# Kernel optimization log

Measured on AMD Instinct MI355X. Metric: run time of the kernel, lower is better.

Reference implementation:

```python
import jax, jax.numpy as jnp
import numpy as np

N_NODES = 100000
N_EDGES = 600000
IN_CH = 128
HID = 64
N_REL = 8


def setup_inputs() -> dict:
    key = jax.random.key(0)
    ks = jax.random.split(key, 9)
    x = jax.random.normal(ks[0], (N_NODES, IN_CH), dtype=jnp.float32)
    edge_index = jax.random.randint(ks[1], (2, N_EDGES), 0, N_NODES)
    edge_type = jax.random.randint(ks[2], (N_EDGES,), 0, N_REL)
    s_in = 1.0 / np.sqrt(IN_CH)   # torch Linear init bound
    s_h = 1.0 / np.sqrt(HID)
    W_rel = jax.random.uniform(ks[3], (N_REL, HID, IN_CH), minval=-s_in, maxval=s_in, dtype=jnp.float32)
    b_rel = jax.random.uniform(ks[4], (N_REL, HID), minval=-s_in, maxval=s_in, dtype=jnp.float32)
    W_self = jax.random.uniform(ks[5], (HID, IN_CH), minval=-s_in, maxval=s_in, dtype=jnp.float32)
    b_self = jax.random.uniform(ks[6], (HID,), minval=-s_in, maxval=s_in, dtype=jnp.float32)
    W_out = jax.random.uniform(ks[7], (1, HID), minval=-s_h, maxval=s_h, dtype=jnp.float32)
    b_out = jax.random.uniform(ks[8], (1,), minval=-s_h, maxval=s_h, dtype=jnp.float32)
    return {"x": x, "edge_index": edge_index, "edge_type": edge_type,
            "W_rel": W_rel, "b_rel": b_rel, "W_self": W_self, "b_self": b_self,
            "W_out": W_out, "b_out": b_out}


def reference(x, edge_index, edge_type, W_rel, b_rel, W_self, b_self, W_out, b_out):
    row, col = edge_index[0], edge_index[1]
    R, H, _ = W_rel.shape
    N = x.shape[0]
    # Project every node under every relation once ([R, N, H]) instead of the
    # per-relation masked gather->GEMM loop: same math (sum over edges of
    # W_{edge_type} x_{src} + b_{edge_type} scattered into dst).
    xp = jnp.einsum('ni,rhi->rnh', x, W_rel)                     # [R, N, H]
    msg = xp.reshape(R * N, H)[edge_type * N + row] + b_rel[edge_type]  # [E, H]
    agg = jax.ops.segment_sum(msg, col, num_segments=N)          # scatter-add into dst
    out = jax.nn.relu(agg + x @ W_self.T + b_self)               # [N, H]
    return (out @ W_out.T + b_out)[:, 0]                          # [N]
```

## Files before the change

### kernel.cpp

```cpp
#include <hip/hip_runtime.h>
#include <hip/hip_bf16.h>

#define IN_CH    128
#define HID      64
#define N_REL    8
#define KSTEP    36
#define SROW2    580
#define SLOT_CAP 64

using bf16x8 = __attribute__((ext_vector_type(8))) short;
using f32x4  = __attribute__((ext_vector_type(4))) float;

__device__ __forceinline__ short f2bf(float f) {
    unsigned int u = __float_as_uint(f);
    u += 0x7fffu + ((u >> 16) & 1u);
    return (short)(u >> 16);
}

__global__ __launch_bounds__(256) void prep_fill_kernel(
    const float* __restrict__ x, unsigned short* __restrict__ xb, int total8,
    const float* __restrict__ W_rel, const float* __restrict__ W_self,
    unsigned short* __restrict__ wpk,
    const int* __restrict__ edge_index, const int* __restrict__ edge_type,
    int* __restrict__ cnt, unsigned int* __restrict__ slots, int E, int nb_xb)
{
    const int b = blockIdx.x, tid = threadIdx.x;
    if (b < nb_xb) {
        int i = b * 256 + tid;
        if (i >= total8) return;
        const float* p = x + (size_t)i * 8;
        float4 a = *(const float4*)p;
        float4 c = *(const float4*)(p + 4);
        bf16x8 o;
        o[0]=f2bf(a.x); o[1]=f2bf(a.y); o[2]=f2bf(a.z); o[3]=f2bf(a.w);
        o[4]=f2bf(c.x); o[5]=f2bf(c.y); o[6]=f2bf(c.z); o[7]=f2bf(c.w);
        *(bf16x8*)(xb + (size_t)i * 8) = o;
    } else if (b < nb_xb + 36) {
        int gid = (b - nb_xb) * 256 + tid;
        int s2   = gid >> 8;
        int t    = (gid >> 6) & 3;
        int lane = gid & 63;
        int h    = t * 16 + (lane & 15);
        int kb   = s2 * 32 + (lane >> 4) * 8;
        bf16x8 o;
        #pragma unroll
        for (int j = 0; j < 8; ++j) {
            int k = kb + j;
            float v = (k < 1024)
                ? W_rel[(size_t)(k >> 7) * HID * IN_CH + (size_t)h * IN_CH + (k & 127)]
                : W_self[(size_t)h * IN_CH + (k - 1024)];
            o[j] = f2bf(v);
        }
        *(bf16x8*)(wpk + (size_t)gid * 8) = o;
    } else {
        int e = (b - nb_xb - 36) * 256 + tid;
        if (e >= E) return;
        int dst = edge_index[E + e];
        unsigned int src = (unsigned int)edge_index[e];
        unsigned int t   = (unsigned int)edge_type[e];
        int pos = atomicAdd(&cnt[dst], 1);
        if (pos < SLOT_CAP)
            slots[(size_t)dst * SLOT_CAP + pos] = (src << 8) | (t << 28);
    }
}

__global__ __launch_bounds__(1024, 8) void rgcn_fused_kernel(
    const unsigned int* __restrict__ xbu,
    const unsigned short* __restrict__ wpk,
    const int* __restrict__ cnt,
    const unsigned int* __restrict__ slots,
    const float* __restrict__ b_rel,
    const float* __restrict__ b_self,
    const float* __restrict__ W_out,
    const float* __restrict__ b_out,
    float* __restrict__ out,
    int N)
{
    __shared__ unsigned int Sb[16 * SROW2];
    __shared__ int cntS[16 * 8];
    const int tid  = threadIdx.x;
    const int wave = tid >> 6;
    const int lane = tid & 63;
    const int l16  = lane & 15;
    const int quad = lane >> 4;
    const int nb   = blockIdx.x * 16;
    const int gnode = nb + wave;

    const unsigned int selfv = xbu[(size_t)gnode * 64 + lane];
    const int rawdeg = cnt[gnode];
    const unsigned int ev = slots[(size_t)gnode * SLOT_CAP + lane];

    #pragma unroll
    for (int k = 0; k < 8; ++k) {
        int idx = k * 1024 + tid;
        Sb[(idx >> 9) * SROW2 + (idx & 511)] = 0;
    }

    const int deg = (rawdeg > SLOT_CAP) ? SLOT_CAP : rawdeg;
    const int myr = (lane < deg) ? (int)(ev >> 28) : 8;
    const unsigned long long below =
        (lane == 63) ? 0x7FFFFFFFFFFFFFFFull : ((1ull << lane) - 1ull);
    int rank = 0, off = 0;
    #pragma unroll
    for (int r = 0; r < 8; ++r) {
        unsigned long long m = __ballot(myr == r);
        int c = __popcll(m);
        if (lane == 0) cntS[wave * 8 + r] = c;
        if (myr == r) rank = off + (int)__popcll(m & below);
        off += c;
    }
    {
        unsigned long long minv = __ballot(myr == 8);
        if (myr == 8) rank = off + (int)__popcll(minv & below);
    }
    const int evs = __builtin_amdgcn_ds_permute(rank << 2, (int)ev);

    __syncthreads();

    {
        const char* xbase = (const char*)xbu + (lane << 2);
        unsigned int* Srow = &Sb[wave * SROW2];
        float s0 = 0.f, s1 = 0.f;
        int cur_r = -1;
        for (int e0 = 0; e0 < deg; e0 += 8) {
            int bn = deg - e0; if (bn > 8) bn = 8;
            unsigned int vv[8], uu[8];
            #pragma unroll
            for (int i = 0; i < 8; ++i) {
                if (i < bn) {
                    vv[i] = (unsigned int)__shfl(evs, e0 + i, 64);
                    uu[i] = *(const unsigned int*)(xbase + (vv[i] & 0x0FFFFFFFu));
                }
            }
            #pragma unroll
            for (int i = 0; i < 8; ++i) {
                if (i >= bn) break;
                const int r = __builtin_amdgcn_readfirstlane((int)(vv[i] >> 28));
                if (r != cur_r) {
                    if (cur_r >= 0) {
                        unsigned int p =
                            ((unsigned int)(unsigned short)f2bf(s1) << 16)
                          | (unsigned int)(unsigned short)f2bf(s0);
                        Srow[cur_r * 64 + lane] = p;
                    }
                    cur_r = r; s0 = 0.f; s1 = 0.f;
                }
                s0 += __uint_as_float(uu[i] << 16);
                s1 += __uint_as_float(uu[i] & 0xffff0000u);
            }
        }
        if (cur_r >= 0) {
            unsigned int p = ((unsigned int)(unsigned short)f2bf(s1) << 16)
                           | (unsigned int)(unsigned short)f2bf(s0);
            Srow[cur_r * 64 + lane] = p;
        }
        Srow[512 + lane] = selfv;
    }
    __syncthreads();

    f32x4 acc[4] = {{0.f,0.f,0.f,0.f},{0.f,0.f,0.f,0.f},
                    {0.f,0.f,0.f,0.f},{0.f,0.f,0.f,0.f}};
    if (wave < 8) {
        const bf16x8* wv = (const bf16x8*)wpk;
        const int s0w = (wave < 4) ? wave * 5 : 20 + (wave - 4) * 4;
        const int ns  = (wave < 4) ? 5 : 4;
        for (int q = 0; q < ns; ++q) {
            const int s2 = s0w + q;
            bf16x8 a[4];
            #pragma unroll
            for (int t = 0; t < 4; ++t)
                a[t] = wv[(size_t)((s2 * 4 + t) * 64) + lane];
            bf16x8 bfrag = *(const bf16x8*)&Sb[l16 * SROW2 + s2 * 16 + quad * 4];
            #pragma unroll
            for (int t = 0; t < 4; ++t)
                acc[t] = __builtin_amdgcn_mfma_f32_16x16x32_bf16(
                    a[t], bfrag, acc[t], 0, 0, 0);
        }
    }
    __syncthreads();

    float* Pf = (float*)Sb;
    if (wave < 8) {
        #pragma unroll
        for (int t = 0; t < 4; ++t)
            *(f32x4*)&Pf[wave * 1100 + l16 * 68 + t * 16 + quad * 4] = acc[t];
    }
    __syncthreads();

    if (tid < 256) {
        const int node = tid & 15, hg = tid >> 4;
        f32x4 v = {0.f, 0.f, 0.f, 0.f};
        #pragma unroll
        for (int w2 = 0; w2 < 8; ++w2)
            v += *(const f32x4*)&Pf[w2 * 1100 + node * 68 + hg * 4];
        float4 bs = *(const float4*)(b_self + hg * 4);
        float4 wo = *(const float4*)(W_out + hg * 4);
        float cb[4] = {0.f, 0.f, 0.f, 0.f};
        #pragma unroll
        for (int r = 0; r < 8; ++r) {
            float cf = (float)cntS[node * 8 + r];
            if (cf != 0.f) {
                float4 br = *(const float4*)(b_rel + r * HID + hg * 4);
                cb[0] += cf * br.x; cb[1] += cf * br.y;
                cb[2] += cf * br.z; cb[3] += cf * br.w;
            }
        }
        float part = 0.f;
        #pragma unroll
        for (int j = 0; j < 4; ++j) {
            float u = v[j] + (&bs.x)[j] + cb[j];
            u = fmaxf(u, 0.f);
            part += u * (&wo.x)[j];
        }
        Pf[8800 + hg * 16 + node] = part;
    }
    __syncthreads();
    if (tid < 16) {
        float sum = 0.f;
        #pragma unroll
        for (int hg = 0; hg < 16; ++hg) sum += Pf[8800 + hg * 16 + tid];
        out[nb + tid] = sum + b_out[0];
    }
}

extern "C" void kernel_launch(void* const* d_in, const int* in_sizes, int n_in,
                              void* d_out, int out_size, void* d_ws, size_t ws_size,
                              hipStream_t stream)
{
    const float* x          = (const float*)d_in[0];
    const int*   edge_index = (const int*)  d_in[1];
    const int*   edge_type  = (const int*)  d_in[2];
    const float* W_rel      = (const float*)d_in[3];
    const float* b_rel      = (const float*)d_in[4];
    const float* W_self     = (const float*)d_in[5];
    const float* b_self     = (const float*)d_in[6];
    const float* W_out      = (const float*)d_in[7];
    const float* b_out      = (const float*)d_in[8];
    float* out = (float*)d_out;

    const int N = in_sizes[0] / IN_CH;
    const int E = in_sizes[2];

    char* w = (char*)d_ws;
    unsigned short* xb  = (unsigned short*)w;  w += (size_t)N * IN_CH * 2;
    unsigned short* wpk = (unsigned short*)w;  w += (size_t)KSTEP * 4 * 64 * 8 * 2;
    int* cnt            = (int*)w;             w += (size_t)N * 4;
    unsigned int* slots = (unsigned int*)w;    w += (size_t)N * SLOT_CAP * 4;

    const int total8 = N * IN_CH / 8;
    const int nb_xb  = (total8 + 255) / 256;
    const int nb_e   = (E + 255) / 256;

    hipMemsetAsync(cnt, 0, (size_t)N * 4, stream);

    prep_fill_kernel<<<nb_xb + 36 + nb_e, 256, 0, stream>>>(
        x, xb, total8, W_rel, W_self, wpk,
        edge_index, edge_type, cnt, slots, E, nb_xb);

    rgcn_fused_kernel<<<N / 16, 1024, 0, stream>>>(
        (const unsigned int*)xb, wpk, cnt, slots,
        b_rel, b_self, W_out, b_out, out, N);
}
```

Baseline: 240.8 us.

## Drop bf16 pre-conversion of x and gather fp32 rows directly

Removes the prep pass that converted all of x to bf16. The fused kernel now gathers neighbor rows as fp32 float2 straight from x and converts the self row to bf16 in-kernel. Slot encoding shifts src by 9 so it becomes a byte offset into 512-byte fp32 rows. Edge loads and slot stores are marked nontemporal. This saves a full read/write pass over x, but each gather now moves twice the bytes, and src<<9 caps the node index at 2^19 before it collides with the type bits.

```diff
diff --git a/kernel.cpp b/kernel.cpp
--- a/kernel.cpp
+++ b/kernel.cpp
@@ -18,25 +18,14 @@
 }
 
 __global__ __launch_bounds__(256) void prep_fill_kernel(
-    const float* __restrict__ x, unsigned short* __restrict__ xb, int total8,
     const float* __restrict__ W_rel, const float* __restrict__ W_self,
     unsigned short* __restrict__ wpk,
     const int* __restrict__ edge_index, const int* __restrict__ edge_type,
-    int* __restrict__ cnt, unsigned int* __restrict__ slots, int E, int nb_xb)
+    int* __restrict__ cnt, unsigned int* __restrict__ slots, int E)
 {
     const int b = blockIdx.x, tid = threadIdx.x;
-    if (b < nb_xb) {
-        int i = b * 256 + tid;
-        if (i >= total8) return;
-        const float* p = x + (size_t)i * 8;
-        float4 a = *(const float4*)p;
-        float4 c = *(const float4*)(p + 4);
-        bf16x8 o;
-        o[0]=f2bf(a.x); o[1]=f2bf(a.y); o[2]=f2bf(a.z); o[3]=f2bf(a.w);
-        o[4]=f2bf(c.x); o[5]=f2bf(c.y); o[6]=f2bf(c.z); o[7]=f2bf(c.w);
-        *(bf16x8*)(xb + (size_t)i * 8) = o;
-    } else if (b < nb_xb + 36) {
-        int gid = (b - nb_xb) * 256 + tid;
+    if (b < 36) {
+        int gid = b * 256 + tid;
         int s2   = gid >> 8;
         int t    = (gid >> 6) & 3;
         int lane = gid & 63;
@@ -53,19 +42,20 @@
         }
         *(bf16x8*)(wpk + (size_t)gid * 8) = o;
     } else {
-        int e = (b - nb_xb - 36) * 256 + tid;
+        int e = (b - 36) * 256 + tid;
         if (e >= E) return;
-        int dst = edge_index[E + e];
-        unsigned int src = (unsigned int)edge_index[e];
-        unsigned int t   = (unsigned int)edge_type[e];
+        int dst = __builtin_nontemporal_load(edge_index + E + e);
+        unsigned int src = (unsigned int)__builtin_nontemporal_load(edge_index + e);
+        unsigned int t   = (unsigned int)__builtin_nontemporal_load(edge_type + e);
         int pos = atomicAdd(&cnt[dst], 1);
         if (pos < SLOT_CAP)
-            slots[(size_t)dst * SLOT_CAP + pos] = (src << 8) | (t << 28);
+            __builtin_nontemporal_store((src << 9) | (t << 28),
+                                        &slots[(size_t)dst * SLOT_CAP + pos]);
     }
 }
 
 __global__ __launch_bounds__(1024, 8) void rgcn_fused_kernel(
-    const unsigned int* __restrict__ xbu,
+    const float* __restrict__ x,
     const unsigned short* __restrict__ wpk,
     const int* __restrict__ cnt,
     const unsigned int* __restrict__ slots,
@@ -86,7 +76,7 @@
     const int nb   = blockIdx.x * 16;
     const int gnode = nb + wave;
 
-    const unsigned int selfv = xbu[(size_t)gnode * 64 + lane];
+    const float2 sf = *(const float2*)((const char*)x + (size_t)gnode * 512 + (lane << 3));
     const int rawdeg = cnt[gnode];
     const unsigned int ev = slots[(size_t)gnode * SLOT_CAP + lane];
 
@@ -118,18 +108,19 @@
     __syncthreads();
 
     {
-        const char* xbase = (const char*)xbu + (lane << 2);
+        const char* xbase = (const char*)x + (lane << 3);
         unsigned int* Srow = &Sb[wave * SROW2];
         float s0 = 0.f, s1 = 0.f;
         int cur_r = -1;
         for (int e0 = 0; e0 < deg; e0 += 8) {
             int bn = deg - e0; if (bn > 8) bn = 8;
-            unsigned int vv[8], uu[8];
+            unsigned int vv[8];
+            float2 uu[8];
             #pragma unroll
             for (int i = 0; i < 8; ++i) {
                 if (i < bn) {
                     vv[i] = (unsigned int)__shfl(evs, e0 + i, 64);
-                    uu[i] = *(const unsigned int*)(xbase + (vv[i] & 0x0FFFFFFFu));
+                    uu[i] = *(const float2*)(xbase + (vv[i] & 0x07FFFFFFu));
                 }
             }
             #pragma unroll
@@ -145,8 +136,8 @@
                     }
                     cur_r = r; s0 = 0.f; s1 = 0.f;
                 }
-                s0 += __uint_as_float(uu[i] << 16);
-                s1 += __uint_as_float(uu[i] & 0xffff0000u);
+                s0 += uu[i].x;
+                s1 += uu[i].y;
             }
         }
         if (cur_r >= 0) {
@@ -154,7 +145,8 @@
                            | (unsigned int)(unsigned short)f2bf(s0);
             Srow[cur_r * 64 + lane] = p;
         }
-        Srow[512 + lane] = selfv;
+        Srow[512 + lane] = ((unsigned int)(unsigned short)f2bf(sf.y) << 16)
+                         | (unsigned int)(unsigned short)f2bf(sf.x);
     }
     __syncthreads();
 
@@ -242,22 +234,17 @@
     const int E = in_sizes[2];
 
     char* w = (char*)d_ws;
-    unsigned short* xb  = (unsigned short*)w;  w += (size_t)N * IN_CH * 2;
     unsigned short* wpk = (unsigned short*)w;  w += (size_t)KSTEP * 4 * 64 * 8 * 2;
     int* cnt            = (int*)w;             w += (size_t)N * 4;
     unsigned int* slots = (unsigned int*)w;    w += (size_t)N * SLOT_CAP * 4;
 
-    const int total8 = N * IN_CH / 8;
-    const int nb_xb  = (total8 + 255) / 256;
-    const int nb_e   = (E + 255) / 256;
+    const int nb_e = (E + 255) / 256;
 
     hipMemsetAsync(cnt, 0, (size_t)N * 4, stream);
 
-    prep_fill_kernel<<<nb_xb + 36 + nb_e, 256, 0, stream>>>(
-        x, xb, total8, W_rel, W_self, wpk,
-        edge_index, edge_type, cnt, slots, E, nb_xb);
+    prep_fill_kernel<<<36 + nb_e, 256, 0, stream>>>(
+        W_rel, W_self, wpk, edge_index, edge_type, cnt, slots, E);
 
     rgcn_fused_kernel<<<N / 16, 1024, 0, stream>>>(
-        (const unsigned int*)xb, wpk, cnt, slots,
-        b_rel, b_self, W_out, b_out, out, N);
-}
+        x, wpk, cnt, slots, b_rel, b_self, W_out, b_out, out, N);
+}
```

New measurement: 263.1 us. 9.3% more time.
